# Kernel tuning notes

Hardware: AMD Instinct MI355X
Metric: run time of the kernel (lower is better)

## Reference

```python
import jax, jax.numpy as jnp
import numpy as np

B, S, H, D = 2, 2048, 32, 128
DM = H * D  # 4096
SCALE = D ** -0.5


def setup_inputs() -> dict:
    key = jax.random.key(0)
    ks = jax.random.split(key, 7)
    std = DM ** -0.5
    return {
        "q": jax.random.normal(ks[0], (B, S, DM), dtype=jnp.float32),
        "k": jax.random.normal(ks[1], (B, S, DM), dtype=jnp.float32),
        "v": jax.random.normal(ks[2], (B, S, DM), dtype=jnp.float32),
        # torch nn.Linear weights are [out_features, in_features]
        "Wq": jax.random.normal(ks[3], (DM, DM), dtype=jnp.float32) * std,
        "Wk": jax.random.normal(ks[4], (DM, DM), dtype=jnp.float32) * std,
        "Wv": jax.random.normal(ks[5], (DM, DM), dtype=jnp.float32) * std,
        "Wo": jax.random.normal(ks[6], (DM, DM), dtype=jnp.float32) * std,
    }


def reference(q, k, v, Wq, Wk, Wv, Wo):
    # Linear: y = x @ W^T (no bias, qkv_bias=False)
    qp = q @ Wq.T  # [B,S,DM]
    kp = k @ Wk.T
    vp = v @ Wv.T
    # [B,S,DM] -> [B,H,S,D]
    qh = qp.reshape(B, S, H, D).transpose(0, 2, 1, 3)
    kh = kp.reshape(B, S, H, D).transpose(0, 2, 1, 3)
    vh = vp.reshape(B, S, H, D).transpose(0, 2, 1, 3)
    # scaled dot-product attention (no mask; attn_mask default None)
    scores = jnp.einsum("bhqd,bhkd->bhqk", qh, kh) * SCALE  # [B,H,S,S]
    probs = jax.nn.softmax(scores, axis=-1)
    ctx = jnp.einsum("bhqk,bhkd->bhqd", probs, vh)  # [B,H,S,D]
    ctx = ctx.transpose(0, 2, 1, 3).reshape(B, S, DM)
    return ctx @ Wo.T  # [B,S,DM]
```

## Files before the change

### kernel.cpp

```cpp
#include <hip/hip_runtime.h>
#include <stdint.h>


using u16 = unsigned short;
using u32 = unsigned int;

typedef __attribute__((ext_vector_type(8))) short bf16x8;
typedef __attribute__((ext_vector_type(8))) u16 u16x8;
typedef __attribute__((ext_vector_type(4))) float f32x4;

#define MFMA_BF16(A, B, C) __builtin_amdgcn_mfma_f32_16x16x32_bf16((A), (B), (C), 0, 0, 0)

static constexpr int kS = 2048, kDM = 4096, kD = 128;
static constexpr size_t kMat = (size_t)4096 * 4096;
static constexpr float kScaleLog2e = 0.08838834764831845f * 1.44269504088896340736f;

static __device__ __forceinline__ void gload_lds16(const u16* g, u16* l) {
  __builtin_amdgcn_global_load_lds((const __attribute__((address_space(1))) void*)g,
                                   (__attribute__((address_space(3))) void*)l, 16, 0, 0);
}

static __device__ __forceinline__ u16 f2bf(float f) {
  u32 u = __float_as_uint(f);
  u32 r = u + 0x7FFFu + ((u >> 16) & 1u);
  return (u16)(r >> 16);
}

static __device__ __forceinline__ u16x8 cvt8(float4 a, float4 b) {
  u16x8 r;
  r[0] = f2bf(a.x); r[1] = f2bf(a.y); r[2] = f2bf(a.z); r[3] = f2bf(a.w);
  r[4] = f2bf(b.x); r[5] = f2bf(b.y); r[6] = f2bf(b.z); r[7] = f2bf(b.w);
  return r;
}

__global__ __launch_bounds__(256) void cvt_kernel(
    const float* __restrict__ s0, const float* __restrict__ s1,
    const float* __restrict__ s2, const float* __restrict__ s3,
    const float* __restrict__ s4, const float* __restrict__ s5,
    const float* __restrict__ s6, u16* __restrict__ dst) {
  const int y = blockIdx.y;
  const float* s = (y == 0) ? s0 : (y == 1) ? s1 : (y == 2) ? s2 : (y == 3) ? s3
                  : (y == 4) ? s4 : (y == 5) ? s5 : s6;
  u16* d = dst + (size_t)y * kMat;
  const size_t nchunk = kMat / 8;
  const size_t step = (size_t)gridDim.x * 256;
  for (size_t c = (size_t)blockIdx.x * 256 + threadIdx.x; c < nchunk; c += step) {
    const float* p = s + c * 8;
    float4 a = *(const float4*)p;
    float4 b = *(const float4*)(p + 4);
    *(u16x8*)(d + c * 8) = cvt8(a, b);
  }
}

template <bool TRANS, bool OUT_F32>
static __device__ __forceinline__ void gemm256(const u16* __restrict__ X,
                                               const u16* __restrict__ W,
                                               void* __restrict__ Yv,
                                               u16* __restrict__ lds) {
  constexpr int NT = kDM / 64;
  const int tid = threadIdx.x;
  const int lane = tid & 63;
  const int w = tid >> 6;
  const int fr = lane & 15;
  const int fq = lane >> 4;
  const int wr = w >> 2;
  const int wc = w & 3;
  const int m0 = blockIdx.y * 256;
  const int n0 = blockIdx.x * 256;

  const int srow = tid >> 3;
  const int scol = ((tid & 7) ^ (srow & 7)) * 8;
  const u16* Xrow = X + (size_t)(m0 + srow) * kDM + scol;
  const u16* Wrow = W + (size_t)(n0 + srow) * kDM + scol;
  const int w512 = w * 512;

  const int rBb = wc * 64 + fr;
  const int rAb = wr * 128 + fr;
  const int swz = fr & 7;

  f32x4 acc[8][4] = {};

#define STAGE2(ROWP, qrow, k0, ldq)                                       \
  do {                                                                    \
    gload_lds16((ROWP) + (size_t)(qrow) * kDM + (k0), &lds[(ldq) + w512]); \
    gload_lds16((ROWP) + (size_t)((qrow) + 64) * kDM + (k0),              \
                &lds[(ldq) + 4096 + w512]);                               \
  } while (0)

  STAGE2(Wrow, 0, 0, 0);
  STAGE2(Wrow, 128, 0, 8192);
  STAGE2(Xrow, 0, 0, 16384);
  STAGE2(Xrow, 128, 0, 24576);
  STAGE2(Wrow, 0, 64, 32768);
  STAGE2(Wrow, 128, 64, 32768 + 8192);
  STAGE2(Xrow, 0, 64, 32768 + 16384);
  asm volatile("s_waitcnt vmcnt(6)" ::: "memory");
  __builtin_amdgcn_s_barrier();

  for (int t = 0; t < NT; ++t) {
    const int d = t & 1;
    const int Boff = d * 32768;
    const int Aoff = Boff + 16384;
    bf16x8 bfr[4][2], af[8][2];

#pragma unroll
    for (int nf = 0; nf < 4; ++nf)
#pragma unroll
      for (int ks = 0; ks < 2; ++ks)
        bfr[nf][ks] = *(const bf16x8*)&lds[Boff + (rBb + nf * 16) * 64 +
                                           (((ks * 4 + fq) ^ swz) * 8)];
#pragma unroll
    for (int mi = 0; mi < 4; ++mi)
#pragma unroll
      for (int ks = 0; ks < 2; ++ks)
        af[mi][ks] = *(const bf16x8*)&lds[Aoff + (rAb + mi * 16) * 64 +
                                          (((ks * 4 + fq) ^ swz) * 8)];
    if (t + 1 < NT) STAGE2(Xrow, 128, (t + 1) * 64, ((t + 1) & 1) * 32768 + 24576);
    __builtin_amdgcn_s_barrier();
    __builtin_amdgcn_s_setprio(1);
#pragma unroll
    for (int mi = 0; mi < 2; ++mi)
#pragma unroll
      for (int nf = 0; nf < 4; ++nf)
#pragma unroll
        for (int ks = 0; ks < 2; ++ks)
          acc[mi][nf] = TRANS ? MFMA_BF16(bfr[nf][ks], af[mi][ks], acc[mi][nf])
                              : MFMA_BF16(af[mi][ks], bfr[nf][ks], acc[mi][nf]);
    __builtin_amdgcn_s_setprio(0);
    __builtin_amdgcn_s_barrier();

#pragma unroll
    for (int mi = 4; mi < 6; ++mi)
#pragma unroll
      for (int ks = 0; ks < 2; ++ks)
        af[mi][ks] = *(const bf16x8*)&lds[Aoff + (rAb + mi * 16) * 64 +
                                          (((ks * 4 + fq) ^ swz) * 8)];
    if (t + 2 < NT) STAGE2(Wrow, 0, (t + 2) * 64, d * 32768 + 0);
    __builtin_amdgcn_s_barrier();
    __builtin_amdgcn_s_setprio(1);
#pragma unroll
    for (int mi = 2; mi < 4; ++mi)
#pragma unroll
      for (int nf = 0; nf < 4; ++nf)
#pragma unroll
        for (int ks = 0; ks < 2; ++ks)
          acc[mi][nf] = TRANS ? MFMA_BF16(bfr[nf][ks], af[mi][ks], acc[mi][nf])
                              : MFMA_BF16(af[mi][ks], bfr[nf][ks], acc[mi][nf]);
    __builtin_amdgcn_s_setprio(0);
    __builtin_amdgcn_s_barrier();

#pragma unroll
    for (int mi = 6; mi < 8; ++mi)
#pragma unroll
      for (int ks = 0; ks < 2; ++ks)
        af[mi][ks] = *(const bf16x8*)&lds[Aoff + (rAb + mi * 16) * 64 +
                                          (((ks * 4 + fq) ^ swz) * 8)];
    if (t + 2 < NT) STAGE2(Wrow, 128, (t + 2) * 64, d * 32768 + 8192);
    __builtin_amdgcn_s_barrier();
    __builtin_amdgcn_s_setprio(1);
#pragma unroll
    for (int mi = 4; mi < 6; ++mi)
#pragma unroll
      for (int nf = 0; nf < 4; ++nf)
#pragma unroll
        for (int ks = 0; ks < 2; ++ks)
          acc[mi][nf] = TRANS ? MFMA_BF16(bfr[nf][ks], af[mi][ks], acc[mi][nf])
                              : MFMA_BF16(af[mi][ks], bfr[nf][ks], acc[mi][nf]);
    __builtin_amdgcn_s_setprio(0);
    asm volatile("s_waitcnt lgkmcnt(0)" ::: "memory");
    __builtin_amdgcn_s_barrier();

    if (t + 2 < NT) STAGE2(Xrow, 0, (t + 2) * 64, d * 32768 + 16384);
    __builtin_amdgcn_s_barrier();
    __builtin_amdgcn_s_setprio(1);
#pragma unroll
    for (int mi = 6; mi < 8; ++mi)
#pragma unroll
      for (int nf = 0; nf < 4; ++nf)
#pragma unroll
        for (int ks = 0; ks < 2; ++ks)
          acc[mi][nf] = TRANS ? MFMA_BF16(bfr[nf][ks], af[mi][ks], acc[mi][nf])
                              : MFMA_BF16(af[mi][ks], bfr[nf][ks], acc[mi][nf]);
    __builtin_amdgcn_s_setprio(0);
    if (t + 2 < NT)
      asm volatile("s_waitcnt vmcnt(6)" ::: "memory");
    else
      asm volatile("s_waitcnt vmcnt(0)" ::: "memory");
    __builtin_amdgcn_s_barrier();
  }
#undef STAGE2

#pragma unroll
  for (int mi = 0; mi < 8; ++mi)
#pragma unroll
    for (int nf = 0; nf < 4; ++nf) {
      int row, col;
      if constexpr (TRANS) {
        row = n0 + wc * 64 + nf * 16 + fq * 4;
        col = m0 + wr * 128 + mi * 16 + fr;
      } else {
        row = m0 + wr * 128 + mi * 16 + fq * 4;
        col = n0 + wc * 64 + nf * 16 + fr;
      }
      if constexpr (OUT_F32) {
        float* yp = (float*)Yv + (size_t)row * kDM + col;
#pragma unroll
        for (int i = 0; i < 4; ++i) yp[(size_t)i * kDM] = acc[mi][nf][i];
      } else {
        u16* yp = (u16*)Yv + (size_t)row * kDM + col;
#pragma unroll
        for (int i = 0; i < 4; ++i) yp[(size_t)i * kDM] = f2bf(acc[mi][nf][i]);
      }
    }
}

__global__ __launch_bounds__(512, 2) void proj_qk256_kernel(const u16* __restrict__ wsb,
                                                            u16* __restrict__ qp,
                                                            u16* __restrict__ kp) {
  __shared__ u16 lds[65536];
  const int z = blockIdx.z;
  gemm256<false, false>(wsb + (size_t)z * kMat, wsb + (size_t)(3 + z) * kMat,
                        z ? kp : qp, lds);
}

__global__ __launch_bounds__(512, 2) void proj_vT256_kernel(const u16* __restrict__ wsb,
                                                            u16* __restrict__ vpT) {
  __shared__ u16 lds[65536];
  gemm256<true, false>(wsb + 2 * kMat, wsb + 5 * kMat, vpT, lds);
}

__global__ __launch_bounds__(512, 2) void out_proj256_kernel(const u16* __restrict__ ctx,
                                                             const u16* __restrict__ Wob,
                                                             float* __restrict__ out) {
  __shared__ u16 lds[65536];
  gemm256<false, true>(ctx, Wob, out, lds);
}

template <bool A_BF16, bool TRANS, bool OUT_F32>
static __device__ __forceinline__ void gemm_conv(const void* Xv, const float* Wf,
                                                 void* Yv, u16* __restrict__ Als,
                                                 u16* __restrict__ Bls) {
  constexpr int KD = 4096;
  const int tid = threadIdx.x;
  const int lane = tid & 63;
  const int w = tid >> 6;
  const int fr = lane & 15;
  const int fq = lane >> 4;
  const int m0 = blockIdx.y * 128;
  const int n0 = blockIdx.x * 128;

  const int r0 = tid >> 2, cc0 = (tid & 3) * 8;
  const int r1 = r0 + 64;
  const int sr = lane >> 2, sc = (lane & 3) * 8;
  const int u0 = w * 2, u1 = w * 2 + 1;

  const u16* Xb = (const u16*)Xv;
  const float* Xf = (const float*)Xv;

  const int wm = (w >> 1) * 64;
  const int wn = (w & 1) * 64;

  f32x4 acc[4][4] = {};

  for (int kt = 0; kt < KD / 32; ++kt) {
    const int ko = kt * 32;
    if constexpr (A_BF16) {
      gload_lds16(Xb + (size_t)(m0 + u0 * 16 + sr) * KD + ko + sc, &Als[u0 * 512]);
      gload_lds16(Xb + (size_t)(m0 + u1 * 16 + sr) * KD + ko + sc, &Als[u1 * 512]);
    } else {
      const float* p0 = Xf + (size_t)(m0 + r0) * KD + ko + cc0;
      const float* p1 = Xf + (size_t)(m0 + r1) * KD + ko + cc0;
      float4 a0 = *(const float4*)(p0);
      float4 a1 = *(const float4*)(p0 + 4);
      float4 a2 = *(const float4*)(p1);
      float4 a3 = *(const float4*)(p1 + 4);
      *(u16x8*)&Als[r0 * 32 + cc0] = cvt8(a0, a1);
      *(u16x8*)&Als[r1 * 32 + cc0] = cvt8(a2, a3);
    }
    {
      const float* p0 = Wf + (size_t)(n0 + r0) * KD + ko + cc0;
      const float* p1 = Wf + (size_t)(n0 + r1) * KD + ko + cc0;
      float4 b0 = *(const float4*)(p0);
      float4 b1 = *(const float4*)(p0 + 4);
      float4 b2 = *(const float4*)(p1);
      float4 b3 = *(const float4*)(p1 + 4);
      *(u16x8*)&Bls[r0 * 32 + cc0] = cvt8(b0, b1);
      *(u16x8*)&Bls[r1 * 32 + cc0] = cvt8(b2, b3);
    }
    __syncthreads();

    bf16x8 af[4], bfv[4];
#pragma unroll
    for (int i = 0; i < 4; ++i)
      af[i] = *(const bf16x8*)&Als[(wm + i * 16 + fr) * 32 + fq * 8];
#pragma unroll
    for (int i = 0; i < 4; ++i)
      bfv[i] = *(const bf16x8*)&Bls[(wn + i * 16 + fr) * 32 + fq * 8];
#pragma unroll
    for (int a = 0; a < 4; ++a)
#pragma unroll
      for (int bb = 0; bb < 4; ++bb) {
        if constexpr (TRANS)
          acc[a][bb] = MFMA_BF16(bfv[a], af[bb], acc[a][bb]);
        else
          acc[a][bb] = MFMA_BF16(af[a], bfv[bb], acc[a][bb]);
      }
    __syncthreads();
  }

#pragma unroll
  for (int a = 0; a < 4; ++a)
#pragma unroll
    for (int bb = 0; bb < 4; ++bb) {
      const int row = TRANS ? (n0 + wn + a * 16 + fq * 4) : (m0 + wm + a * 16 + fq * 4);
      const int col = TRANS ? (m0 + wm + bb * 16 + fr) : (n0 + wn + bb * 16 + fr);
      if constexpr (OUT_F32) {
        float* yp = (float*)Yv + (size_t)row * kDM + col;
#pragma unroll
        for (int i = 0; i < 4; ++i) yp[(size_t)i * kDM] = acc[a][bb][i];
      } else {
        u16* yp = (u16*)Yv + (size_t)row * kDM + col;
#pragma unroll
        for (int i = 0; i < 4; ++i) yp[(size_t)i * kDM] = f2bf(acc[a][bb][i]);
      }
    }
}

__global__ __launch_bounds__(256) void proj_qk_conv_kernel(
    const float* __restrict__ q, const float* __restrict__ k,
    const float* __restrict__ Wq, const float* __restrict__ Wk,
    u16* __restrict__ qp, u16* __restrict__ kp) {
  __shared__ u16 Als[128 * 32];
  __shared__ u16 Bls[128 * 32];
  const int z = blockIdx.z;
  gemm_conv<false, false, false>(z ? k : q, z ? Wk : Wq, z ? kp : qp, Als, Bls);
}

__global__ __launch_bounds__(256) void proj_vT_conv_kernel(
    const float* __restrict__ v, const float* __restrict__ Wv, u16* __restrict__ vpT) {
  __shared__ u16 Als[128 * 32];
  __shared__ u16 Bls[128 * 32];
  gemm_conv<false, true, false>(v, Wv, vpT, Als, Bls);
}

__global__ __launch_bounds__(256) void out_proj_conv_kernel(const u16* __restrict__ ctx,
                                                            const float* __restrict__ Wo,
                                                            float* __restrict__ out) {
  __shared__ u16 Als[128 * 32];
  __shared__ u16 Bls[128 * 32];
  gemm_conv<true, false, true>(ctx, Wo, out, Als, Bls);
}

__global__ __launch_bounds__(256) void attn_kernel(const u16* __restrict__ qp,
                                                   const u16* __restrict__ kp,
                                                   const u16* __restrict__ vpT,
                                                   u16* __restrict__ ctx) {
  constexpr int KB = 64;
  constexpr int PST = 72;

  __shared__ u16 Kls[KB * 128];
  __shared__ u16 Vt[kD * KB];
  __shared__ u16 Pls[4][2 * 16 * PST];

  const int tid = threadIdx.x, lane = tid & 63, w = tid >> 6;
  const int fr = lane & 15, fq = lane >> 4;
  const int bh = blockIdx.y;
  const int b = bh >> 5, h = bh & 31;
  const int q0 = blockIdx.x * 128;

  const u16* qbase = qp + ((size_t)b * kS) * kDM + h * kD;
  const u16* kbase = kp + ((size_t)b * kS) * kDM + h * kD;
  const u16* vtbase = vpT + (size_t)(h * kD) * kDM + b * kS;

  bf16x8 qf[2][4];
#pragma unroll
  for (int rb = 0; rb < 2; ++rb)
#pragma unroll
    for (int kc = 0; kc < 4; ++kc)
      qf[rb][kc] = *(const bf16x8*)(qbase + (size_t)(q0 + w * 32 + rb * 16 + fr) * kDM +
                                    kc * 32 + fq * 8);

  f32x4 oacc[2][8] = {};
  float mrun[2][4], lrun[2][4];
#pragma unroll
  for (int rb = 0; rb < 2; ++rb)
#pragma unroll
    for (int i = 0; i < 4; ++i) {
      mrun[rb][i] = -1e30f;
      lrun[rb][i] = 0.f;
    }

  const int krl = lane >> 4;
  const int kdp = lane & 15;
  const int vdl = lane >> 3;
  const int vc = lane & 7;

  for (int kt = 0; kt < kS / KB; ++kt) {
    const int kr0 = kt * KB;
#pragma unroll
    for (int t = 0; t < 4; ++t) {
      const int u = w * 4 + t;
      const int r = u * 4 + krl;
      const int dps = kdp ^ (r & 7);
      gload_lds16(kbase + (size_t)(kr0 + r) * kDM + dps * 8, &Kls[u * 512]);
    }
#pragma unroll
    for (int t = 0; t < 4; ++t) {
      const int u = w * 4 + t;
      const int d = u * 8 + vdl;
      gload_lds16(vtbase + (size_t)d * kDM + kr0 + ((vc ^ (d & 7)) * 8), &Vt[u * 512]);
    }
    __syncthreads();

    f32x4 sacc[2][4] = {};
#pragma unroll
    for (int cb = 0; cb < 4; ++cb) {
      const int n = cb * 16 + fr;
      bf16x8 kf[4];
#pragma unroll
      for (int kc = 0; kc < 4; ++kc) {
        const int d0 = kc * 4 + fq;
        kf[kc] = *(const bf16x8*)&Kls[n * 128 + (d0 ^ (n & 7)) * 8];
      }
#pragma unroll
      for (int rb = 0; rb < 2; ++rb)
#pragma unroll
        for (int kc = 0; kc < 4; ++kc)
          sacc[rb][cb] = MFMA_BF16(qf[rb][kc], kf[kc], sacc[rb][cb]);
    }

#pragma unroll
    for (int rb = 0; rb < 2; ++rb) {
      float s2[4][4];
#pragma unroll
      for (int cb = 0; cb < 4; ++cb)
#pragma unroll
        for (int i = 0; i < 4; ++i) s2[cb][i] = sacc[rb][cb][i] * kScaleLog2e;
      float mt[4];
#pragma unroll
      for (int i = 0; i < 4; ++i)
        mt[i] = fmaxf(fmaxf(s2[0][i], s2[1][i]), fmaxf(s2[2][i], s2[3][i]));
#pragma unroll
      for (int off = 1; off < 16; off <<= 1)
#pragma unroll
        for (int i = 0; i < 4; ++i) mt[i] = fmaxf(mt[i], __shfl_xor(mt[i], off));

      float scl[4], rsum[4];
#pragma unroll
      for (int i = 0; i < 4; ++i) {
        const float mnew = fmaxf(mrun[rb][i], mt[i]);
        scl[i] = exp2f(mrun[rb][i] - mnew);
        mrun[rb][i] = mnew;
        rsum[i] = 0.f;
      }
#pragma unroll
      for (int cb = 0; cb < 4; ++cb)
#pragma unroll
        for (int i = 0; i < 4; ++i) {
          const float p = exp2f(s2[cb][i] - mrun[rb][i]);
          rsum[i] += p;
          Pls[w][rb * (16 * PST) + (fq * 4 + i) * PST + cb * 16 + fr] = f2bf(p);
        }
#pragma unroll
      for (int off = 1; off < 16; off <<= 1)
#pragma unroll
        for (int i = 0; i < 4; ++i) rsum[i] += __shfl_xor(rsum[i], off);
#pragma unroll
      for (int i = 0; i < 4; ++i) lrun[rb][i] = lrun[rb][i] * scl[i] + rsum[i];
#pragma unroll
      for (int db = 0; db < 8; ++db)
#pragma unroll
        for (int i = 0; i < 4; ++i) oacc[rb][db][i] *= scl[i];
    }

    asm volatile("s_waitcnt lgkmcnt(0)" ::: "memory");

    bf16x8 pf[2][2];
#pragma unroll
    for (int rb = 0; rb < 2; ++rb)
#pragma unroll
      for (int kb = 0; kb < 2; ++kb)
        pf[rb][kb] = *(const bf16x8*)&Pls[w][rb * (16 * PST) + fr * PST + kb * 32 + fq * 8];
#pragma unroll
    for (int db = 0; db < 8; ++db) {
      const int d = db * 16 + fr;
      bf16x8 vf0 = *(const bf16x8*)&Vt[d * KB + ((fq ^ (d & 7)) << 3)];
      bf16x8 vf1 = *(const bf16x8*)&Vt[d * KB + (((4 + fq) ^ (d & 7)) << 3)];
#pragma unroll
      for (int rb = 0; rb < 2; ++rb) {
        oacc[rb][db] = MFMA_BF16(pf[rb][0], vf0, oacc[rb][db]);
        oacc[rb][db] = MFMA_BF16(pf[rb][1], vf1, oacc[rb][db]);
      }
    }
    __syncthreads();
  }

  u16* cbase = ctx + ((size_t)b * kS) * kDM + h * kD;
#pragma unroll
  for (int rb = 0; rb < 2; ++rb) {
    float inv[4];
#pragma unroll
    for (int i = 0; i < 4; ++i) inv[i] = 1.0f / lrun[rb][i];
#pragma unroll
    for (int db = 0; db < 8; ++db)
#pragma unroll
      for (int i = 0; i < 4; ++i) {
        const int row = q0 + w * 32 + rb * 16 + fq * 4 + i;
        const int col = db * 16 + fr;
        cbase[(size_t)row * kDM + col] = f2bf(oacc[rb][db][i] * inv[i]);
      }
  }
}

extern "C" void kernel_launch(void* const* d_in, const int* in_sizes, int n_in,
                              void* d_out, int out_size, void* d_ws, size_t ws_size,
                              hipStream_t stream) {
  const float* q = (const float*)d_in[0];
  const float* k = (const float*)d_in[1];
  const float* v = (const float*)d_in[2];
  const float* Wq = (const float*)d_in[3];
  const float* Wk = (const float*)d_in[4];
  const float* Wv = (const float*)d_in[5];
  const float* Wo = (const float*)d_in[6];
  float* out = (float*)d_out;

  const size_t needFast = 11 * kMat * sizeof(u16);

  if (ws_size >= needFast) {
    u16* wsb = (u16*)d_ws;
    u16* qp = wsb + 7 * kMat;
    u16* kp = wsb + 8 * kMat;
    u16* vpT = wsb + 9 * kMat;
    u16* ctx = wsb + 10 * kMat;

    cvt_kernel<<<dim3(1024, 7), 256, 0, stream>>>(q, k, v, Wq, Wk, Wv, Wo, wsb);
    proj_qk256_kernel<<<dim3(16, 16, 2), 512, 0, stream>>>(wsb, qp, kp);
    proj_vT256_kernel<<<dim3(16, 16), 512, 0, stream>>>(wsb, vpT);
    attn_kernel<<<dim3(16, 64), 256, 0, stream>>>(qp, kp, vpT, ctx);
    out_proj256_kernel<<<dim3(16, 16), 512, 0, stream>>>(ctx, wsb + 6 * kMat, out);
  } else {
    u16* qp = (u16*)d_ws;
    u16* kp = qp + kMat;
    u16* vpT = kp + kMat;
    u16* ctx = vpT + kMat;

    proj_qk_conv_kernel<<<dim3(32, 32, 2), 256, 0, stream>>>(q, k, Wq, Wk, qp, kp);
    proj_vT_conv_kernel<<<dim3(32, 32), 256, 0, stream>>>(v, Wv, vpT);
    attn_kernel<<<dim3(16, 64), 256, 0, stream>>>(qp, kp, vpT, ctx);
    out_proj_conv_kernel<<<dim3(32, 32, 1), 256, 0, stream>>>(ctx, Wo, out);
  }
}
```

Baseline: 878.2 us.

## Fold softmax scale into Q, lazy rescale, and widen attention blocks

```diff
diff --git a/kernel.cpp b/kernel.cpp
--- a/kernel.cpp
+++ b/kernel.cpp
@@ -1,4 +1,5 @@
 #include <hip/hip_runtime.h>
+#include <hip/hip_bf16.h>
 #include <stdint.h>
 
 
@@ -24,6 +25,16 @@
   u32 u = __float_as_uint(f);
   u32 r = u + 0x7FFFu + ((u >> 16) & 1u);
   return (u16)(r >> 16);
+}
+
+static __device__ __forceinline__ float bf2f(u16 x) {
+  return __uint_as_float((u32)x << 16);
+}
+
+static __device__ __forceinline__ u16 nbf(float f) {
+  union { __hip_bfloat16 h; u16 u; } cv;
+  cv.h = __float2bfloat16(f);
+  return cv.u;
 }
 
 static __device__ __forceinline__ u16x8 cvt8(float4 a, float4 b) {
@@ -351,22 +362,23 @@
   gemm_conv<true, false, true>(ctx, Wo, out, Als, Bls);
 }
 
-__global__ __launch_bounds__(256) void attn_kernel(const u16* __restrict__ qp,
+__global__ __launch_bounds__(512) void attn_kernel(const u16* __restrict__ qp,
                                                    const u16* __restrict__ kp,
                                                    const u16* __restrict__ vpT,
                                                    u16* __restrict__ ctx) {
   constexpr int KB = 64;
   constexpr int PST = 72;
+  constexpr float THR = 11.5f;
 
   __shared__ u16 Kls[KB * 128];
   __shared__ u16 Vt[kD * KB];
-  __shared__ u16 Pls[4][2 * 16 * PST];
+  __shared__ u16 Pls[8][2 * 16 * PST];
 
   const int tid = threadIdx.x, lane = tid & 63, w = tid >> 6;
   const int fr = lane & 15, fq = lane >> 4;
   const int bh = blockIdx.y;
   const int b = bh >> 5, h = bh & 31;
-  const int q0 = blockIdx.x * 128;
+  const int q0 = blockIdx.x * 256;
 
   const u16* qbase = qp + ((size_t)b * kS) * kDM + h * kD;
   const u16* kbase = kp + ((size_t)b * kS) * kDM + h * kD;
@@ -376,9 +388,14 @@
 #pragma unroll
   for (int rb = 0; rb < 2; ++rb)
 #pragma unroll
-    for (int kc = 0; kc < 4; ++kc)
-      qf[rb][kc] = *(const bf16x8*)(qbase + (size_t)(q0 + w * 32 + rb * 16 + fr) * kDM +
-                                    kc * 32 + fq * 8);
+    for (int kc = 0; kc < 4; ++kc) {
+      const u16x8 raw = *(const u16x8*)(qbase +
+          (size_t)(q0 + w * 32 + rb * 16 + fr) * kDM + kc * 32 + fq * 8);
+      bf16x8 s;
+#pragma unroll
+      for (int j = 0; j < 8; ++j) s[j] = (short)f2bf(bf2f(raw[j]) * kScaleLog2e);
+      qf[rb][kc] = s;
+    }
 
   f32x4 oacc[2][8] = {};
   float mrun[2][4], lrun[2][4];
@@ -398,15 +415,15 @@
   for (int kt = 0; kt < kS / KB; ++kt) {
     const int kr0 = kt * KB;
 #pragma unroll
-    for (int t = 0; t < 4; ++t) {
-      const int u = w * 4 + t;
+    for (int t = 0; t < 2; ++t) {
+      const int u = w * 2 + t;
       const int r = u * 4 + krl;
       const int dps = kdp ^ (r & 7);
       gload_lds16(kbase + (size_t)(kr0 + r) * kDM + dps * 8, &Kls[u * 512]);
     }
 #pragma unroll
-    for (int t = 0; t < 4; ++t) {
-      const int u = w * 4 + t;
+    for (int t = 0; t < 2; ++t) {
+      const int u = w * 2 + t;
       const int d = u * 8 + vdl;
       gload_lds16(vtbase + (size_t)d * kDM + kr0 + ((vc ^ (d & 7)) * 8), &Vt[u * 512]);
     }
@@ -422,55 +439,59 @@
         const int d0 = kc * 4 + fq;
         kf[kc] = *(const bf16x8*)&Kls[n * 128 + (d0 ^ (n & 7)) * 8];
       }
+      __builtin_amdgcn_s_setprio(1);
 #pragma unroll
       for (int rb = 0; rb < 2; ++rb)
 #pragma unroll
         for (int kc = 0; kc < 4; ++kc)
           sacc[rb][cb] = MFMA_BF16(qf[rb][kc], kf[kc], sacc[rb][cb]);
+      __builtin_amdgcn_s_setprio(0);
     }
 
 #pragma unroll
     for (int rb = 0; rb < 2; ++rb) {
-      float s2[4][4];
+      float mt[4];
+#pragma unroll
+      for (int i = 0; i < 4; ++i)
+        mt[i] = fmaxf(fmaxf(sacc[rb][0][i], sacc[rb][1][i]),
+                      fmaxf(sacc[rb][2][i], sacc[rb][3][i]));
+#pragma unroll
+      for (int off = 1; off < 16; off <<= 1)
+#pragma unroll
+        for (int i = 0; i < 4; ++i) mt[i] = fmaxf(mt[i], __shfl_xor(mt[i], off));
+
+      const float grow = fmaxf(fmaxf(mt[0] - mrun[rb][0], mt[1] - mrun[rb][1]),
+                               fmaxf(mt[2] - mrun[rb][2], mt[3] - mrun[rb][3]));
+      if (__any(grow > THR)) {
+        float scl[4];
+#pragma unroll
+        for (int i = 0; i < 4; ++i) {
+          const float mnew = fmaxf(mrun[rb][i], mt[i]);
+          scl[i] = exp2f(mrun[rb][i] - mnew);
+          mrun[rb][i] = mnew;
+          lrun[rb][i] *= scl[i];
+        }
+#pragma unroll
+        for (int db = 0; db < 8; ++db)
+#pragma unroll
+          for (int i = 0; i < 4; ++i) oacc[rb][db][i] *= scl[i];
+      }
+
+      float rsum[4] = {0.f, 0.f, 0.f, 0.f};
 #pragma unroll
       for (int cb = 0; cb < 4; ++cb)
 #pragma unroll
-        for (int i = 0; i < 4; ++i) s2[cb][i] = sacc[rb][cb][i] * kScaleLog2e;
-      float mt[4];
-#pragma unroll
-      for (int i = 0; i < 4; ++i)
-        mt[i] = fmaxf(fmaxf(s2[0][i], s2[1][i]), fmaxf(s2[2][i], s2[3][i]));
+        for (int i = 0; i < 4; ++i) {
+          const float p = exp2f(sacc[rb][cb][i] - mrun[rb][i]);
+          rsum[i] += p;
+          Pls[w][rb * (16 * PST) + (fq * 4 + i) * PST + cb * 16 + fr] = nbf(p);
+        }
 #pragma unroll
       for (int off = 1; off < 16; off <<= 1)
 #pragma unroll
-        for (int i = 0; i < 4; ++i) mt[i] = fmaxf(mt[i], __shfl_xor(mt[i], off));
-
-      float scl[4], rsum[4];
-#pragma unroll
-      for (int i = 0; i < 4; ++i) {
-        const float mnew = fmaxf(mrun[rb][i], mt[i]);
-        scl[i] = exp2f(mrun[rb][i] - mnew);
-        mrun[rb][i] = mnew;
-        rsum[i] = 0.f;
-      }
-#pragma unroll
-      for (int cb = 0; cb < 4; ++cb)
-#pragma unroll
-        for (int i = 0; i < 4; ++i) {
-          const float p = exp2f(s2[cb][i] - mrun[rb][i]);
-          rsum[i] += p;
-          Pls[w][rb * (16 * PST) + (fq * 4 + i) * PST + cb * 16 + fr] = f2bf(p);
-        }
-#pragma unroll
-      for (int off = 1; off < 16; off <<= 1)
-#pragma unroll
         for (int i = 0; i < 4; ++i) rsum[i] += __shfl_xor(rsum[i], off);
 #pragma unroll
-      for (int i = 0; i < 4; ++i) lrun[rb][i] = lrun[rb][i] * scl[i] + rsum[i];
-#pragma unroll
-      for (int db = 0; db < 8; ++db)
-#pragma unroll
-        for (int i = 0; i < 4; ++i) oacc[rb][db][i] *= scl[i];
+      for (int i = 0; i < 4; ++i) lrun[rb][i] += rsum[i];
     }
 
     asm volatile("s_waitcnt lgkmcnt(0)" ::: "memory");
@@ -486,11 +507,13 @@
       const int d = db * 16 + fr;
       bf16x8 vf0 = *(const bf16x8*)&Vt[d * KB + ((fq ^ (d & 7)) << 3)];
       bf16x8 vf1 = *(const bf16x8*)&Vt[d * KB + (((4 + fq) ^ (d & 7)) << 3)];
+      __builtin_amdgcn_s_setprio(1);
 #pragma unroll
       for (int rb = 0; rb < 2; ++rb) {
         oacc[rb][db] = MFMA_BF16(pf[rb][0], vf0, oacc[rb][db]);
         oacc[rb][db] = MFMA_BF16(pf[rb][1], vf1, oacc[rb][db]);
       }
+      __builtin_amdgcn_s_setprio(0);
     }
     __syncthreads();
   }
@@ -507,7 +530,7 @@
       for (int i = 0; i < 4; ++i) {
         const int row = q0 + w * 32 + rb * 16 + fq * 4 + i;
         const int col = db * 16 + fr;
-        cbase[(size_t)row * kDM + col] = f2bf(oacc[rb][db][i] * inv[i]);
+        cbase[(size_t)row * kDM + col] = nbf(oacc[rb][db][i] * inv[i]);
       }
   }
 }
@@ -536,7 +559,7 @@
     cvt_kernel<<<dim3(1024, 7), 256, 0, stream>>>(q, k, v, Wq, Wk, Wv, Wo, wsb);
     proj_qk256_kernel<<<dim3(16, 16, 2), 512, 0, stream>>>(wsb, qp, kp);
     proj_vT256_kernel<<<dim3(16, 16), 512, 0, stream>>>(wsb, vpT);
-    attn_kernel<<<dim3(16, 64), 256, 0, stream>>>(qp, kp, vpT, ctx);
+    attn_kernel<<<dim3(8, 64), 512, 0, stream>>>(qp, kp, vpT, ctx);
     out_proj256_kernel<<<dim3(16, 16), 512, 0, stream>>>(ctx, wsb + 6 * kMat, out);
   } else {
     u16* qp = (u16*)d_ws;
@@ -546,7 +569,7 @@
 
     proj_qk_conv_kernel<<<dim3(32, 32, 2), 256, 0, stream>>>(q, k, Wq, Wk, qp, kp);
     proj_vT_conv_kernel<<<dim3(32, 32), 256, 0, stream>>>(v, Wv, vpT);
-    attn_kernel<<<dim3(16, 64), 256, 0, stream>>>(qp, kp, vpT, ctx);
+    attn_kernel<<<dim3(8, 64), 512, 0, stream>>>(qp, kp, vpT, ctx);
     out_proj_conv_kernel<<<dim3(32, 32, 1), 256, 0, stream>>>(ctx, Wo, out);
   }
 }
```

Result: faster. 830.4 us (-5.4%).
